# Kernel optimization log

Measured on AMD Instinct MI355X. Metric: run time of the kernel, lower is better.

The kernel has to match this reference:

```python
import jax, jax.numpy as jnp
import numpy as np

N, DIM, DK, DV = 8192, 1024, 128, 128


def setup_inputs() -> dict:
    key = jax.random.key(0)
    ks = jax.random.split(key, 5)
    # Match equinox Linear init scale roughly (uniform(-1/sqrt(in), 1/sqrt(in)))
    lim = 1.0 / np.sqrt(DIM)
    return {
        "x": jax.random.normal(ks[0], (N, DIM), dtype=jnp.float32),
        "Wqk": jax.random.uniform(ks[1], (DK, DIM), jnp.float32, -lim, lim),
        "bqk": jax.random.uniform(ks[2], (DK,), jnp.float32, -lim, lim),
        "Wv": jax.random.uniform(ks[3], (DV, DIM), jnp.float32, -lim, lim),
        "bv": jax.random.uniform(ks[4], (DV,), jnp.float32, -lim, lim),
    }


def reference(x, Wqk, bqk, Wv, bv):
    # shared QK projection: q == k == x @ Wqk^T + bqk  -> [n, dk]
    qk = jnp.einsum("nd,kd->nk", x, Wqk) + bqk
    v = jnp.einsum("nd,vd->nv", x, Wv) + bv  # [n, dv]
    # full n x n score matrix (no 1/sqrt(dk) scaling in the original)
    score = jnp.einsum("ik,jk->ij", qk, qk)  # [n, n]
    score = jax.nn.softmax(score, axis=-1)
    return jnp.einsum("ij,jv->iv", score, v)  # [n, dv]
```

## Files before the change

kernel.cpp:

```cpp
#include <hip/hip_runtime.h>
#include <math.h>

#define NROWS 8192
#define DIMX  1024
#define DKV   128
#define KSPLIT 4
#define KEYS_PER_SPLIT (NROWS / KSPLIT)
#define BN 64
#define QK_SCALE 1.2011224087864498f
#define M_FIX 96.0f

typedef __attribute__((ext_vector_type(8))) short bf16x8;
typedef __attribute__((ext_vector_type(4))) short s16x4;
typedef __attribute__((ext_vector_type(4))) float f32x4;

static __device__ __forceinline__ short f2bf(float f) {
    union { float f; unsigned u; } v; v.f = f;
    unsigned r = v.u + 0x7fff + ((v.u >> 16) & 1);
    return (short)(r >> 16);
}

__global__ __launch_bounds__(256) void wcvt_kernel(
    const float* __restrict__ Wqk, const float* __restrict__ bqk,
    const float* __restrict__ Wv,  const float* __restrict__ bv,
    short* __restrict__ wb, float* __restrict__ bb)
{
    const int idx = blockIdx.x * 1024 + threadIdx.x * 4;
    const bool isqk = idx < DKV * DIMX;
    const float* src = isqk ? (Wqk + idx) : (Wv + (idx - DKV * DIMX));
    const float sc = isqk ? QK_SCALE : 1.0f;
    const float4 f = *(const float4*)src;
    s16x4 o;
    o.x = f2bf(f.x * sc); o.y = f2bf(f.y * sc);
    o.z = f2bf(f.z * sc); o.w = f2bf(f.w * sc);
    *(s16x4*)&wb[idx] = o;
    if (blockIdx.x == 0) {
        const int t = threadIdx.x;
        bb[t] = (t < DKV) ? bqk[t] * QK_SCALE : bv[t - DKV];
    }
}

__global__ __launch_bounds__(256) void proj_kernel(
    const float* __restrict__ x, const short* __restrict__ wb,
    const float* __restrict__ bb, short* __restrict__ qkb, short* __restrict__ vtb)
{
    __shared__ __align__(16) short xb[32 * 1024];

    const int tid  = threadIdx.x;
    const int lane = tid & 63;
    const int wave = tid >> 6;
    const int l15  = lane & 15;
    const int quad = lane >> 4;
    const int mat  = blockIdx.y;
    const int rbase = blockIdx.x * 32;
    const int wr = wave >> 1, wc = wave & 1;
    const short* wsrc = wb + (size_t)mat * DKV * DIMX;

    #pragma unroll 8
    for (int i = 0; i < 32; ++i) {
        const float4 f = *(const float4*)(x + (size_t)(rbase + i) * DIMX + tid * 4);
        s16x4 o;
        o.x = f2bf(f.x); o.y = f2bf(f.y); o.z = f2bf(f.z); o.w = f2bf(f.w);
        *(s16x4*)&xb[i * 1024 + ((tid * 4) ^ ((i & 7) << 3))] = o;
    }
    __syncthreads();

    f32x4 acc[4];
    for (int i = 0; i < 4; ++i) acc[i] = (f32x4)0.0f;

    const int arow = wr * 16 + l15;
    const int aswz = (arow & 7) << 3;
    const short* arowp = &xb[arow * 1024];

    #pragma unroll 2
    for (int kk = 0; kk < 32; ++kk) {
        const bf16x8 a = *(const bf16x8*)&arowp[(kk * 32 + quad * 8) ^ aswz];
        for (int nt = 0; nt < 4; ++nt) {
            const int col = wc * 64 + nt * 16 + l15;
            const bf16x8 b = *(const bf16x8*)(wsrc + (size_t)col * DIMX + kk * 32 + quad * 8);
            acc[nt] = __builtin_amdgcn_mfma_f32_16x16x32_bf16(a, b, acc[nt], 0, 0, 0);
        }
    }

    const int rw = rbase + wr * 16 + quad * 4;
    for (int nt = 0; nt < 4; ++nt) {
        const int col = wc * 64 + nt * 16 + l15;
        const float bias = bb[mat * DKV + col];
        if (mat == 0) {
            for (int r = 0; r < 4; ++r)
                qkb[(size_t)(rw + r) * DKV + col] = f2bf(acc[nt][r] + bias);
        } else {
            s16x4 o;
            o.x = f2bf(acc[nt][0] + bias); o.y = f2bf(acc[nt][1] + bias);
            o.z = f2bf(acc[nt][2] + bias); o.w = f2bf(acc[nt][3] + bias);
            *(s16x4*)&vtb[(size_t)col * NROWS + rw] = o;
        }
    }
}

__global__ __launch_bounds__(256, 2) void flash_kernel(
    const short* __restrict__ qkb, const short* __restrict__ vtb,
    float* __restrict__ opart, float* __restrict__ lpart)
{
    __shared__ __align__(16) short kt[2][64 * 128];
    __shared__ __align__(16) short vt[2][128 * 64];
    __shared__ __align__(16) short pb[4 * 16 * 64];

    const int tid  = threadIdx.x;
    const int lane = tid & 63;
    const int wave = tid >> 6;
    const int l15  = lane & 15;
    const int quad = lane >> 4;
    const int rbase = blockIdx.x * 64 + wave * 16;
    const int ks = blockIdx.y;
    const int swzr = (l15 & 7) << 3;

    unsigned koff[4], voff[4];
    for (int i = 0; i < 4; ++i) {
        const int krow = wave * 16 + i * 4 + quad;
        koff[i] = (unsigned)krow * 256u
                + (((unsigned)l15 * 16u) ^ (((unsigned)krow & 7u) << 4));
        const int vrow = wave * 32 + i * 8 + (lane >> 3);
        voff[i] = (unsigned)vrow * (unsigned)(NROWS * 2)
                + ((((unsigned)lane & 7u) * 16u) ^ (((unsigned)vrow & 7u) << 4));
    }

#define FL_ISSUE(buf, j0) do { \
        const char* kb_ = (const char*)qkb + (size_t)(j0) * (DKV * 2); \
        const char* vb_ = (const char*)vtb + (size_t)(j0) * 2; \
        for (int i = 0; i < 4; ++i) \
            __builtin_amdgcn_global_load_lds( \
                (const __attribute__((address_space(1))) void*)(kb_ + koff[i]), \
                (__attribute__((address_space(3))) void*)((char*)&kt[buf][0] + (wave * 4 + i) * 1024), \
                16, 0, 0); \
        for (int i = 0; i < 4; ++i) \
            __builtin_amdgcn_global_load_lds( \
                (const __attribute__((address_space(1))) void*)(vb_ + voff[i]), \
                (__attribute__((address_space(3))) void*)((char*)&vt[buf][0] + (wave * 4 + i) * 1024), \
                16, 0, 0); \
    } while (0)

    bf16x8 qf[4];
    {
        const short* qrow = qkb + (size_t)(rbase + l15) * DKV;
        for (int k = 0; k < 4; ++k)
            qf[k] = *(const bf16x8*)(qrow + k * 32 + quad * 8);
    }

    f32x4 oacc[8];
    for (int i = 0; i < 8; ++i) oacc[i] = (f32x4)0.0f;
    float lacc[4] = {0.f, 0.f, 0.f, 0.f};

    const int j_begin = ks * KEYS_PER_SPLIT;
    short* pw = &pb[wave * 1024];

    FL_ISSUE(0, j_begin);
    __syncthreads();

    int cur = 0;
    for (int j0 = j_begin; j0 < j_begin + KEYS_PER_SPLIT; j0 += BN) {
        const bool more = (j0 + BN) < (j_begin + KEYS_PER_SPLIT);
        if (more) FL_ISSUE(cur ^ 1, j0 + BN);

        f32x4 s[4];
        __builtin_amdgcn_s_setprio(1);
        for (int nt = 0; nt < 4; ++nt) {
            f32x4 acc = (f32x4)0.0f;
            for (int k = 0; k < 4; ++k) {
                const bf16x8 b = *(const bf16x8*)
                    &kt[cur][(nt * 16 + l15) * 128 + ((k * 32 + quad * 8) ^ swzr)];
                acc = __builtin_amdgcn_mfma_f32_16x16x32_bf16(qf[k], b, acc, 0, 0, 0);
            }
            s[nt] = acc;
        }
        __builtin_amdgcn_s_setprio(0);

        for (int nt = 0; nt < 4; ++nt)
            for (int r = 0; r < 4; ++r)
                s[nt][r] = exp2f(s[nt][r] - M_FIX);
        for (int r = 0; r < 4; ++r)
            lacc[r] += (s[0][r] + s[1][r]) + (s[2][r] + s[3][r]);

        for (int r = 0; r < 4; ++r) {
            const int row = quad * 4 + r;
            unsigned pk01, pk23;
            asm("v_cvt_pk_bf16_f32 %0, %1, %2" : "=v"(pk01) : "v"(s[0][r]), "v"(s[1][r]));
            asm("v_cvt_pk_bf16_f32 %0, %1, %2" : "=v"(pk23) : "v"(s[2][r]), "v"(s[3][r]));
            short* prow = &pw[row * 64];
            const int sw = (row & 7) << 3;
            prow[(0 * 16 + l15) ^ sw] = (short)pk01;
            prow[(1 * 16 + l15) ^ sw] = (short)(pk01 >> 16);
            prow[(2 * 16 + l15) ^ sw] = (short)pk23;
            prow[(3 * 16 + l15) ^ sw] = (short)(pk23 >> 16);
        }

        __builtin_amdgcn_s_setprio(1);
        for (int kk = 0; kk < 2; ++kk) {
            const bf16x8 a = *(const bf16x8*)&pw[l15 * 64 + ((kk * 32 + quad * 8) ^ swzr)];
            for (int nt = 0; nt < 8; ++nt) {
                const bf16x8 b = *(const bf16x8*)
                    &vt[cur][(nt * 16 + l15) * 64 + ((kk * 32 + quad * 8) ^ swzr)];
                oacc[nt] = __builtin_amdgcn_mfma_f32_16x16x32_bf16(a, b, oacc[nt], 0, 0, 0);
            }
        }
        __builtin_amdgcn_s_setprio(0);

        __syncthreads();
        cur ^= 1;
    }

    for (int r = 0; r < 4; ++r)
        for (int off = 1; off < 16; off <<= 1)
            lacc[r] += __shfl_xor(lacc[r], off);

    const int rw = rbase + quad * 4;
    for (int nt = 0; nt < 8; ++nt) {
        const int col = nt * 16 + l15;
        for (int r = 0; r < 4; ++r)
            opart[((size_t)ks * NROWS + rw + r) * DKV + col] = oacc[nt][r];
    }
    if (l15 == 0)
        for (int r = 0; r < 4; ++r)
            lpart[ks * NROWS + rw + r] = lacc[r];
#undef FL_ISSUE
}

__global__ __launch_bounds__(256) void combine_kernel(
    const float* __restrict__ opart, const float* __restrict__ lpart,
    float* __restrict__ out)
{
    const int idx = blockIdx.x * 256 + threadIdx.x;
    const int row = idx >> 7;
    float L = 0.f, acc = 0.f;
    for (int s = 0; s < KSPLIT; ++s) {
        L   += lpart[s * NROWS + row];
        acc += opart[(size_t)s * NROWS * DKV + idx];
    }
    out[idx] = acc / L;
}

extern "C" void kernel_launch(void* const* d_in, const int* in_sizes, int n_in,
                              void* d_out, int out_size, void* d_ws, size_t ws_size,
                              hipStream_t stream) {
    const float* x   = (const float*)d_in[0];
    const float* Wqk = (const float*)d_in[1];
    const float* bqk = (const float*)d_in[2];
    const float* Wv  = (const float*)d_in[3];
    const float* bv  = (const float*)d_in[4];
    float* out = (float*)d_out;

    char* ws = (char*)d_ws;
    short* qkb   = (short*)ws;
    short* vtb   = (short*)(ws + (2u << 20));
    short* wb    = (short*)(ws + (4u << 20));
    float* bb    = (float*)(ws + (4u << 20) + (512u << 10));
    float* opart = (float*)(ws + (5u << 20));
    float* lpart = (float*)(ws + (21u << 20));

    wcvt_kernel<<<dim3(256), 256, 0, stream>>>(Wqk, bqk, Wv, bv, wb, bb);
    proj_kernel<<<dim3(256, 2), 256, 0, stream>>>(x, wb, bb, qkb, vtb);
    flash_kernel<<<dim3(NROWS / 64, KSPLIT), 256, 0, stream>>>(qkb, vtb, opart, lpart);
    combine_kernel<<<dim3(NROWS * DKV / 256), 256, 0, stream>>>(opart, lpart, out);
}
```

Baseline: 175.6 us.

## Split waves into row-pairs by key half with LDS reduction and MFMA row sums

Each wave now handles 32 query rows over half of the 64-key tile instead of 16 rows over all keys, so each K and V fragment read from LDS feeds two MFMAs. The two key-half partial outputs are reduced through LDS at the end. Row sums of P are now computed with an MFMA against a ones vector rather than VALU adds and shuffles, which also means they are summed from the bf16-rounded P. The cost is twice the accumulator registers per wave (16 f32x4 for O), which may pressure occupancy under launch_bounds(256,2), plus an extra epilogue reduction.

```diff
diff --git a/kernel.cpp b/kernel.cpp
--- a/kernel.cpp
+++ b/kernel.cpp
@@ -104,16 +104,19 @@
 {
     __shared__ __align__(16) short kt[2][64 * 128];
     __shared__ __align__(16) short vt[2][128 * 64];
-    __shared__ __align__(16) short pb[4 * 16 * 64];
+    __shared__ __align__(16) short pb[4][32 * 64];
 
     const int tid  = threadIdx.x;
     const int lane = tid & 63;
     const int wave = tid >> 6;
     const int l15  = lane & 15;
     const int quad = lane >> 4;
-    const int rbase = blockIdx.x * 64 + wave * 16;
+    const int rg   = wave >> 1;
+    const int kh   = wave & 1;
+    const int rbase = blockIdx.x * 64 + rg * 32;
     const int ks = blockIdx.y;
     const int swzr = (l15 & 7) << 3;
+    const int swzp = (l15 & 12) << 2;
 
     unsigned koff[4], voff[4];
     for (int i = 0; i < 4; ++i) {
@@ -140,19 +143,25 @@
                 16, 0, 0); \
     } while (0)
 
-    bf16x8 qf[4];
-    {
-        const short* qrow = qkb + (size_t)(rbase + l15) * DKV;
+    bf16x8 qf[2][4];
+    #pragma unroll 2
+    for (int h = 0; h < 2; ++h) {
+        const short* qrow = qkb + (size_t)(rbase + h * 16 + l15) * DKV;
         for (int k = 0; k < 4; ++k)
-            qf[k] = *(const bf16x8*)(qrow + k * 32 + quad * 8);
-    }
-
-    f32x4 oacc[8];
-    for (int i = 0; i < 8; ++i) oacc[i] = (f32x4)0.0f;
-    float lacc[4] = {0.f, 0.f, 0.f, 0.f};
+            qf[h][k] = *(const bf16x8*)(qrow + k * 32 + quad * 8);
+    }
+
+    bf16x8 ones;
+    for (int j = 0; j < 8; ++j) ones[j] = (short)0x3F80;
+
+    f32x4 oacc[2][8];
+    #pragma unroll 2
+    for (int h = 0; h < 2; ++h)
+        for (int i = 0; i < 8; ++i) oacc[h][i] = (f32x4)0.0f;
+    f32x4 lsum[2] = {(f32x4)0.0f, (f32x4)0.0f};
 
     const int j_begin = ks * KEYS_PER_SPLIT;
-    short* pw = &pb[wave * 1024];
+    short* pw = &pb[wave][0];
 
     FL_ISSUE(0, j_begin);
     __syncthreads();
@@ -162,45 +171,49 @@
         const bool more = (j0 + BN) < (j_begin + KEYS_PER_SPLIT);
         if (more) FL_ISSUE(cur ^ 1, j0 + BN);
 
-        f32x4 s[4];
+        f32x4 s[2][2];
         __builtin_amdgcn_s_setprio(1);
-        for (int nt = 0; nt < 4; ++nt) {
-            f32x4 acc = (f32x4)0.0f;
+        #pragma unroll 2
+        for (int ntl = 0; ntl < 2; ++ntl) {
+            f32x4 a0 = (f32x4)0.0f, a1 = (f32x4)0.0f;
             for (int k = 0; k < 4; ++k) {
                 const bf16x8 b = *(const bf16x8*)
-                    &kt[cur][(nt * 16 + l15) * 128 + ((k * 32 + quad * 8) ^ swzr)];
-                acc = __builtin_amdgcn_mfma_f32_16x16x32_bf16(qf[k], b, acc, 0, 0, 0);
-            }
-            s[nt] = acc;
+                    &kt[cur][(kh * 32 + ntl * 16 + l15) * 128 + ((k * 32 + quad * 8) ^ swzr)];
+                a0 = __builtin_amdgcn_mfma_f32_16x16x32_bf16(qf[0][k], b, a0, 0, 0, 0);
+                a1 = __builtin_amdgcn_mfma_f32_16x16x32_bf16(qf[1][k], b, a1, 0, 0, 0);
+            }
+            s[0][ntl] = a0; s[1][ntl] = a1;
         }
         __builtin_amdgcn_s_setprio(0);
 
-        for (int nt = 0; nt < 4; ++nt)
-            for (int r = 0; r < 4; ++r)
-                s[nt][r] = exp2f(s[nt][r] - M_FIX);
-        for (int r = 0; r < 4; ++r)
-            lacc[r] += (s[0][r] + s[1][r]) + (s[2][r] + s[3][r]);
-
-        for (int r = 0; r < 4; ++r) {
-            const int row = quad * 4 + r;
-            unsigned pk01, pk23;
-            asm("v_cvt_pk_bf16_f32 %0, %1, %2" : "=v"(pk01) : "v"(s[0][r]), "v"(s[1][r]));
-            asm("v_cvt_pk_bf16_f32 %0, %1, %2" : "=v"(pk23) : "v"(s[2][r]), "v"(s[3][r]));
-            short* prow = &pw[row * 64];
-            const int sw = (row & 7) << 3;
-            prow[(0 * 16 + l15) ^ sw] = (short)pk01;
-            prow[(1 * 16 + l15) ^ sw] = (short)(pk01 >> 16);
-            prow[(2 * 16 + l15) ^ sw] = (short)pk23;
-            prow[(3 * 16 + l15) ^ sw] = (short)(pk23 >> 16);
-        }
+        #pragma unroll 2
+        for (int h = 0; h < 2; ++h)
+            for (int ntl = 0; ntl < 2; ++ntl)
+                for (int r = 0; r < 4; ++r)
+                    s[h][ntl][r] = exp2f(s[h][ntl][r] - M_FIX);
+
+        #pragma unroll 2
+        for (int h = 0; h < 2; ++h)
+            for (int r = 0; r < 4; ++r) {
+                const int row = h * 16 + quad * 4 + r;
+                unsigned pk;
+                asm("v_cvt_pk_bf16_f32 %0, %1, %2" : "=v"(pk) : "v"(s[h][0][r]), "v"(s[h][1][r]));
+                const int sw = quad << 4;
+                pw[row * 64 + ((l15) ^ sw)]      = (short)pk;
+                pw[row * 64 + ((16 + l15) ^ sw)] = (short)(pk >> 16);
+            }
 
         __builtin_amdgcn_s_setprio(1);
-        for (int kk = 0; kk < 2; ++kk) {
-            const bf16x8 a = *(const bf16x8*)&pw[l15 * 64 + ((kk * 32 + quad * 8) ^ swzr)];
+        {
+            const bf16x8 a0 = *(const bf16x8*)&pw[(l15) * 64 + ((quad * 8) ^ swzp)];
+            const bf16x8 a1 = *(const bf16x8*)&pw[(16 + l15) * 64 + ((quad * 8) ^ swzp)];
+            lsum[0] = __builtin_amdgcn_mfma_f32_16x16x32_bf16(a0, ones, lsum[0], 0, 0, 0);
+            lsum[1] = __builtin_amdgcn_mfma_f32_16x16x32_bf16(a1, ones, lsum[1], 0, 0, 0);
             for (int nt = 0; nt < 8; ++nt) {
                 const bf16x8 b = *(const bf16x8*)
-                    &vt[cur][(nt * 16 + l15) * 64 + ((kk * 32 + quad * 8) ^ swzr)];
-                oacc[nt] = __builtin_amdgcn_mfma_f32_16x16x32_bf16(a, b, oacc[nt], 0, 0, 0);
+                    &vt[cur][(nt * 16 + l15) * 64 + ((kh * 32 + quad * 8) ^ swzr)];
+                oacc[0][nt] = __builtin_amdgcn_mfma_f32_16x16x32_bf16(a0, b, oacc[0][nt], 0, 0, 0);
+                oacc[1][nt] = __builtin_amdgcn_mfma_f32_16x16x32_bf16(a1, b, oacc[1][nt], 0, 0, 0);
             }
         }
         __builtin_amdgcn_s_setprio(0);
@@ -209,19 +222,37 @@
         cur ^= 1;
     }
 
-    for (int r = 0; r < 4; ++r)
-        for (int off = 1; off < 16; off <<= 1)
-            lacc[r] += __shfl_xor(lacc[r], off);
-
-    const int rw = rbase + quad * 4;
-    for (int nt = 0; nt < 8; ++nt) {
-        const int col = nt * 16 + l15;
-        for (int r = 0; r < 4; ++r)
-            opart[((size_t)ks * NROWS + rw + r) * DKV + col] = oacc[nt][r];
-    }
-    if (l15 == 0)
-        for (int r = 0; r < 4; ++r)
-            lpart[ks * NROWS + rw + r] = lacc[r];
+    float* obuf = (float*)&kt[rg][0];
+    float* lbuf = (float*)&vt[0][0];
+    __syncthreads();
+    if (kh == 1) {
+        #pragma unroll 2
+        for (int h = 0; h < 2; ++h) {
+            for (int nt = 0; nt < 8; ++nt)
+                for (int r = 0; r < 4; ++r)
+                    obuf[(h * 16 + quad * 4 + r) * 128 + nt * 16 + l15] = oacc[h][nt][r];
+            if (l15 == 0)
+                for (int r = 0; r < 4; ++r)
+                    lbuf[rg * 32 + h * 16 + quad * 4 + r] = lsum[h][r];
+        }
+    }
+    __syncthreads();
+    if (kh == 0) {
+        #pragma unroll 2
+        for (int h = 0; h < 2; ++h) {
+            const int rw = rbase + h * 16 + quad * 4;
+            for (int nt = 0; nt < 8; ++nt) {
+                const int col = nt * 16 + l15;
+                for (int r = 0; r < 4; ++r)
+                    opart[((size_t)ks * NROWS + rw + r) * DKV + col] =
+                        oacc[h][nt][r] + obuf[(h * 16 + quad * 4 + r) * 128 + col];
+            }
+            if (l15 == 0)
+                for (int r = 0; r < 4; ++r)
+                    lpart[ks * NROWS + rw + r] =
+                        lsum[h][r] + lbuf[rg * 32 + h * 16 + quad * 4 + r];
+        }
+    }
 #undef FL_ISSUE
 }
 
```

New measurement: 174.3 us. Within noise of the previous version (-0.7%).
